# Kernel optimization log

Measured on AMD Instinct MI355X. Metric: run time of the kernel, lower is better.

Reference implementation:

```python
import jax, jax.numpy as jnp
import numpy as np
import math

D_MODEL = 2048
NUM_HEADS = 16
HEAD_DIM = D_MODEL // NUM_HEADS
B, QLEN, CACHE_LEN = 4, 512, 3584

def setup_inputs() -> dict:
    key = jax.random.key(0)
    ks = jax.random.split(key, 13)
    s = 0.02
    return {
        'query': jax.random.normal(ks[0], (B, QLEN, D_MODEL), jnp.float32),
        'key': jax.random.normal(ks[1], (B, QLEN, D_MODEL), jnp.float32),
        'value': jax.random.normal(ks[2], (B, QLEN, D_MODEL), jnp.float32),
        'cached_k': jax.random.normal(ks[3], (B, CACHE_LEN, D_MODEL), jnp.float32),
        'cached_v': jax.random.normal(ks[4], (B, CACHE_LEN, D_MODEL), jnp.float32),
        'wq': jax.random.normal(ks[5], (D_MODEL, D_MODEL), jnp.float32) * s,
        'bq': jnp.zeros((D_MODEL,), jnp.float32),
        'wk': jax.random.normal(ks[6], (D_MODEL, D_MODEL), jnp.float32) * s,
        'bk': jnp.zeros((D_MODEL,), jnp.float32),
        'wv': jax.random.normal(ks[7], (D_MODEL, D_MODEL), jnp.float32) * s,
        'bv': jnp.zeros((D_MODEL,), jnp.float32),
        'wo': jax.random.normal(ks[8], (D_MODEL, D_MODEL), jnp.float32) * s,
        'bo': jnp.zeros((D_MODEL,), jnp.float32),
    }

def _split_heads(x):
    b, s, _ = x.shape
    return x.reshape(b, s, NUM_HEADS, HEAD_DIM).transpose(0, 2, 1, 3)  # [b,h,s,d]

def reference(query, key, value, cached_k, cached_v, wq, bq, wk, bk, wv, bv, wo, bo):
    # projections (torch Linear: x @ W^T + b)
    Q = query @ wq.T + bq
    K_new = key @ wk.T + bk
    V_new = value @ wv.T + bv
    K = jnp.concatenate([cached_k, K_new], axis=1)  # [b, total, d_model]
    V = jnp.concatenate([cached_v, V_new], axis=1)
    seq_len = query.shape[1]
    total_len = K.shape[1]
    cache_len = total_len - seq_len
    Qh = _split_heads(Q)  # [b,h,q,d]
    Kh = _split_heads(K)  # [b,h,t,d]
    Vh = _split_heads(V)
    scale = math.sqrt(HEAD_DIM)
    scores = jnp.einsum('bhqd,bhtd->bhqt', Qh, Kh) / scale
    # causal mask with cache offset: query i attends to keys j <= cache_len + i
    q_idx = jnp.arange(seq_len)[:, None]
    k_idx = jnp.arange(total_len)[None, :]
    mask = k_idx > (q_idx + cache_len)  # True = masked
    scores = jnp.where(mask[None, None], -jnp.inf, scores)
    attn = jax.nn.softmax(scores, axis=-1)
    out = jnp.einsum('bhqt,bhtd->bhqd', attn, Vh)
    out = out.transpose(0, 2, 1, 3).reshape(query.shape[0], seq_len, D_MODEL)
    out = out @ wo.T + bo
    return out
```

## Files before the change

### kernel.cpp

```cpp
#include <hip/hip_runtime.h>

typedef _Float16 half8 __attribute__((ext_vector_type(8)));
typedef _Float16 half4v __attribute__((ext_vector_type(4)));
typedef float f32x4 __attribute__((ext_vector_type(4)));

#define NB 4
#define SQ 512
#define CL 3584
#define TT 4096
#define DM 2048
#define NH 16
#define DH 128

#define KSW(row, col) ((((row) * 128) + (col)) ^ ((((row) & 7) << 3)))
#define VSW(row, col) ((((row) * 64) + (col)) ^ ((((row) & 7) << 3)))
#define PSW(row, col) ((((row) * 64) + (col)) ^ ((((row) & 7) << 3)))

__device__ __forceinline__ void gl_lds16(const void* g, void* l) {
  __builtin_amdgcn_global_load_lds(
      (const __attribute__((address_space(1))) unsigned int*)g,
      (__attribute__((address_space(3))) unsigned int*)l, 16, 0, 0);
}

__global__ __launch_bounds__(256) void cvt_f16(
    const float* __restrict__ s0, const float* __restrict__ s1, const float* __restrict__ s2,
    _Float16* __restrict__ d0, _Float16* __restrict__ d1, _Float16* __restrict__ d2,
    int dstride)
{
  const float* s = blockIdx.y == 0 ? s0 : blockIdx.y == 1 ? s1 : s2;
  _Float16* d = blockIdx.y == 0 ? d0 : blockIdx.y == 1 ? d1 : d2;
  const int n4 = DM * DM / 4;
  for (int v = blockIdx.x * blockDim.x + threadIdx.x; v < n4;
       v += gridDim.x * blockDim.x) {
    float4 x = ((const float4*)s)[v];
    half4v h = { (_Float16)x.x, (_Float16)x.y, (_Float16)x.z, (_Float16)x.w };
    const int m = v >> 9, c = (v << 2) & 2047;
    *(half4v*)&d[(size_t)m * dstride + c] = h;
  }
}

__global__ __launch_bounds__(256) void convert_K(
    const float* __restrict__ ck, _Float16* __restrict__ K)
{
  const long long nvec = (long long)NB * CL * DM / 4;
  const int pb = CL * DM / 4;
  for (long long v = (long long)blockIdx.x * blockDim.x + threadIdx.x; v < nvec;
       v += (long long)gridDim.x * blockDim.x) {
    int b = (int)(v / pb);
    long long r = v - (long long)b * pb;
    float4 x = ((const float4*)ck)[v];
    half4v hx = { (_Float16)x.x, (_Float16)x.y, (_Float16)x.z, (_Float16)x.w };
    ((half4v*)K)[(long long)b * (TT * DM / 4) + r] = hx;
  }
}

__global__ __launch_bounds__(256) void transpose_V(
    const float* __restrict__ cv, _Float16* __restrict__ Vt)
{
  __shared__ _Float16 T[64][72];
  const int t0 = blockIdx.x * 64;
  const int dm0 = blockIdx.y * 64;
  const int b = blockIdx.z;
  const int tid = threadIdx.x;
  {
    const int tr = tid >> 2, c0 = (tid & 3) * 16;
    const float* src = cv + ((size_t)b * CL + t0 + tr) * DM + dm0 + c0;
    float4 a0 = ((const float4*)src)[0];
    float4 a1 = ((const float4*)src)[1];
    float4 a2 = ((const float4*)src)[2];
    float4 a3 = ((const float4*)src)[3];
    half8 h0 = { (_Float16)a0.x, (_Float16)a0.y, (_Float16)a0.z, (_Float16)a0.w,
                 (_Float16)a1.x, (_Float16)a1.y, (_Float16)a1.z, (_Float16)a1.w };
    half8 h1 = { (_Float16)a2.x, (_Float16)a2.y, (_Float16)a2.z, (_Float16)a2.w,
                 (_Float16)a3.x, (_Float16)a3.y, (_Float16)a3.z, (_Float16)a3.w };
    *(half8*)&T[tr][c0] = h0;
    *(half8*)&T[tr][c0 + 8] = h1;
  }
  __syncthreads();
  {
    const int dl = tid >> 2, tc = (tid & 3) * 16;
    const int h = dm0 >> 7, d = (dm0 & 127) + dl;
    half8 o0, o1;
#pragma unroll
    for (int i = 0; i < 8; ++i) o0[i] = T[tc + i][dl];
#pragma unroll
    for (int i = 0; i < 8; ++i) o1[i] = T[tc + 8 + i][dl];
    _Float16* dst = Vt + ((size_t)(b * NH + h) * DH + d) * TT + t0 + tc;
    *(half8*)dst = o0;
    *(half8*)(dst + 8) = o1;
  }
}

template<int MODE>
__global__ __launch_bounds__(512, 4) void mm16(
    const _Float16* __restrict__ A0, const _Float16* __restrict__ A1,
    const _Float16* __restrict__ A2, int astride,
    const _Float16* __restrict__ W0, const _Float16* __restrict__ W1,
    const _Float16* __restrict__ W2,
    const float* __restrict__ b0, const float* __restrict__ b1,
    const float* __restrict__ b2,
    _Float16* __restrict__ Qp, _Float16* __restrict__ Kc,
    _Float16* __restrict__ Vt, float* __restrict__ Co)
{
  __shared__ __align__(16) char smem[4 * 8192];
  char* Abuf = smem;
  char* Wbuf = smem + 2 * 8192;

  const int tid = threadIdx.x;
  const int bm = blockIdx.x, bn = blockIdx.y, z = blockIdx.z;
  const _Float16* Ain = z == 0 ? A0 : z == 1 ? A1 : A2;
  const _Float16* W   = z == 0 ? W0 : z == 1 ? W1 : W2;
  const float* bias   = z == 0 ? b0 : z == 1 ? b1 : b2;

  const int wid = tid >> 6, lane = tid & 63;
  const int wm = wid >> 2, wn = wid & 3;
  const int lr = lane & 15, lg = lane >> 4;

  f32x4 acc[4][2];
#pragma unroll
  for (int i = 0; i < 4; ++i)
#pragma unroll
    for (int j = 0; j < 2; ++j) acc[i][j] = (f32x4){0.f, 0.f, 0.f, 0.f};

  size_t aoff, woff;
  {
    const int o = wid * 1024 + lane * 16;
    const int prow = o >> 7, pb = o & 127;
    const int lb = pb ^ ((prow & 7) << 4);
    const int r = (prow << 1) | (lb >> 6), c = lb & 63;
    aoff = (size_t)(bm * 128 + r) * astride + c;
    woff = (size_t)(bn * 128 + r) * 4096 + c;
  }

  auto stage = [&](int kt, int buf) {
    gl_lds16((const char*)Ain + aoff + kt * 64, Abuf + buf * 8192 + wid * 1024);
    gl_lds16((const char*)W + woff + kt * 64, Wbuf + buf * 8192 + wid * 1024);
  };

  auto lds_addr = [](const char* base, int r, int cb) -> const char* {
    return base + ((r >> 1) << 7) + ((((r & 1) << 6) | cb) ^ (((r >> 1) & 7) << 4));
  };

  auto compute = [&](int buf) {
    const char* ab = Abuf + buf * 8192;
    const char* wb = Wbuf + buf * 8192;
    half8 af[4], bf[2];
#pragma unroll
    for (int i = 0; i < 4; ++i)
      af[i] = *(const half8*)lds_addr(ab, wm * 64 + i * 16 + lr, lg << 4);
#pragma unroll
    for (int j = 0; j < 2; ++j)
      bf[j] = *(const half8*)lds_addr(wb, wn * 32 + j * 16 + lr, lg << 4);
#pragma unroll
    for (int i = 0; i < 4; ++i)
#pragma unroll
      for (int j = 0; j < 2; ++j)
        acc[i][j] = __builtin_amdgcn_mfma_f32_16x16x32_f16(af[i], bf[j], acc[i][j], 0, 0, 0);
  };

  const int NKT = DM / 32;
  stage(0, 0);
  __syncthreads();
  for (int kt = 0; kt < NKT; ++kt) {
    if (kt + 1 < NKT) stage(kt + 1, (kt + 1) & 1);
    compute(kt & 1);
    __syncthreads();
  }

  const float qscale = 0.08838834764831845f * 1.4426950408889634f;
#pragma unroll
  for (int i = 0; i < 4; ++i) {
    const int m0 = bm * 128 + wm * 64 + i * 16 + lg * 4;
#pragma unroll
    for (int j = 0; j < 2; ++j) {
      const int gn = bn * 128 + wn * 32 + j * 16 + lr;
      const float bb = bias[gn];
      if constexpr (MODE == 1) {
#pragma unroll
        for (int r = 0; r < 4; ++r)
          Co[(size_t)(m0 + r) * DM + gn] = acc[i][j][r] + bb;
      } else {
        if (z == 0) {
#pragma unroll
          for (int r = 0; r < 4; ++r)
            Qp[(size_t)(m0 + r) * DM + gn] = (_Float16)((acc[i][j][r] + bb) * qscale);
        } else if (z == 1) {
          const int b = m0 >> 9;
#pragma unroll
          for (int r = 0; r < 4; ++r)
            Kc[((size_t)b * TT + CL + ((m0 + r) & 511)) * DM + gn] =
                (_Float16)(acc[i][j][r] + bb);
        } else {
          half4v hv;
#pragma unroll
          for (int r = 0; r < 4; ++r) hv[r] = (_Float16)(acc[i][j][r] + bb);
          const int b = m0 >> 9, t = CL + (m0 & 511);
          const int h = gn >> 7, d = gn & 127;
          *(half4v*)&Vt[((size_t)(b * NH + h) * DH + d) * TT + t] = hv;
        }
      }
    }
  }
}

__global__ __launch_bounds__(512) void attn_kernel(
    const _Float16* __restrict__ Qp, const _Float16* __restrict__ Kc,
    const _Float16* __restrict__ Vt, _Float16* __restrict__ O0,
    _Float16* __restrict__ O1, float2* __restrict__ ml)
{
  __shared__ _Float16 Ks[2][64 * 128];
  __shared__ _Float16 VTs[3][128 * 64];
  __shared__ _Float16 Ps[8][32 * 64];

  const int tid = threadIdx.x;
  const int lin = blockIdx.x;
  const int xcd = lin & 7, slot = lin >> 3;
  const int pair = xcd * 8 + (slot >> 2);
  const int rem = slot & 3;
  const int qb = rem >> 1, part = rem & 1;
  const int b = pair >> 4, h = pair & 15;

  const int wid = tid >> 6, lane = tid & 63;
  const int lr = lane & 15, lg = lane >> 4;
  const int qw = qb * 256 + wid * 32;

  half8 qf[2][4];
#pragma unroll
  for (int qs = 0; qs < 2; ++qs)
#pragma unroll
    for (int kk = 0; kk < 4; ++kk)
      qf[qs][kk] = *(const half8*)&Qp[(size_t)(b * SQ + qw + qs * 16 + lr) * DM +
                                      h * DH + kk * 32 + lg * 8];

  f32x4 zero = {0.f, 0.f, 0.f, 0.f};
  f32x4 acc[8][2];
#pragma unroll
  for (int d = 0; d < 8; ++d)
#pragma unroll
    for (int qs = 0; qs < 2; ++qs) acc[d][qs] = zero;
  float m_run[2] = {-1e30f, -1e30f}, l_run[2] = {0.f, 0.f};

  const int nt_full = (CL + qb * 256 + 256) / 64;
  const int halfn = nt_full >> 1;
  const int tbeg = part ? halfn : 0;
  const int nt = part ? (nt_full - halfn) : halfn;

  int ksrc[2], vsrc[2];
#pragma unroll
  for (int c = 0; c < 2; ++c) {
    const int p = c * 512 + wid * 64 + lane;
    { const int r = p >> 4, pg = p & 15, gc = pg ^ (r & 7);
      ksrc[c] = r * DM + gc * 8; }
    { const int d = p >> 3, pg = p & 7, gt = pg ^ (d & 7);
      vsrc[c] = d * TT + gt * 8; }
  }
  const _Float16* Kb = Kc + (size_t)b * TT * DM + h * DH;
  const _Float16* Vb = Vt + (size_t)(b * NH + h) * DH * TT;

  auto stage = [&](int tt, int kbuf, int vbuf) {
    const int t0 = (tbeg + tt) * 64;
#pragma unroll
    for (int c = 0; c < 2; ++c)
      gl_lds16(Kb + (size_t)t0 * DM + ksrc[c], &Ks[kbuf][(c * 512 + wid * 64) * 8]);
#pragma unroll
    for (int c = 0; c < 2; ++c)
      gl_lds16(Vb + t0 + vsrc[c], &VTs[vbuf][(c * 512 + wid * 64) * 8]);
  };

  auto qk = [&](int kbuf, f32x4 (*s)[2]) {
#pragma unroll
    for (int j = 0; j < 4; ++j)
#pragma unroll
      for (int qs = 0; qs < 2; ++qs) s[j][qs] = zero;
#pragma unroll
    for (int kk = 0; kk < 4; ++kk)
#pragma unroll
      for (int j = 0; j < 4; ++j) {
        half8 kb = *(const half8*)&Ks[kbuf][KSW(j * 16 + lr, kk * 32 + lg * 8)];
        s[j][0] = __builtin_amdgcn_mfma_f32_16x16x32_f16(kb, qf[0][kk], s[j][0], 0, 0, 0);
        s[j][1] = __builtin_amdgcn_mfma_f32_16x16x32_f16(kb, qf[1][kk], s[j][1], 0, 0, 0);
      }
  };

  auto mask_s = [&](int t0, f32x4 (*s)[2]) {
    if (t0 + 63 > CL + qw) {
#pragma unroll
      for (int j = 0; j < 4; ++j)
#pragma unroll
        for (int qs = 0; qs < 2; ++qs)
#pragma unroll
          for (int r = 0; r < 4; ++r)
            if (t0 + j * 16 + lg * 4 + r > CL + qw + qs * 16 + lr) s[j][qs][r] = -1e30f;
    }
  };

  auto softmax_step = [&](f32x4 (*s)[2]) {
    float mt[2];
#pragma unroll
    for (int qs = 0; qs < 2; ++qs) {
      float m = s[0][qs][0];
#pragma unroll
      for (int j = 0; j < 4; ++j)
#pragma unroll
        for (int r = 0; r < 4; ++r) m = fmaxf(m, s[j][qs][r]);
      mt[qs] = m;
    }
    if (!__all(mt[0] <= m_run[0] + 10.0f && mt[1] <= m_run[1] + 10.0f)) {
#pragma unroll
      for (int qs = 0; qs < 2; ++qs) {
        float m = fmaxf(mt[qs], __shfl_xor(mt[qs], 16));
        m = fmaxf(m, __shfl_xor(m, 32));
        const float mn = fmaxf(m_run[qs], m);
        const float fsc = exp2f(m_run[qs] - mn);
        m_run[qs] = mn;
        l_run[qs] *= fsc;
#pragma unroll
        for (int d = 0; d < 8; ++d)
#pragma unroll
          for (int r = 0; r < 4; ++r) acc[d][qs][r] *= fsc;
      }
    }
#pragma unroll
    for (int qs = 0; qs < 2; ++qs) {
      float ps = 0.f;
#pragma unroll
      for (int j = 0; j < 4; ++j) {
        float p0 = exp2f(s[j][qs][0] - m_run[qs]);
        float p1 = exp2f(s[j][qs][1] - m_run[qs]);
        float p2 = exp2f(s[j][qs][2] - m_run[qs]);
        float p3 = exp2f(s[j][qs][3] - m_run[qs]);
        ps += (p0 + p1) + (p2 + p3);
        half4v hp = { (_Float16)p0, (_Float16)p1, (_Float16)p2, (_Float16)p3 };
        *(half4v*)&Ps[wid][PSW(qs * 16 + lr, j * 16 + lg * 4)] = hp;
      }
      l_run[qs] += ps;
    }
  };

  auto pv = [&](int vbuf) {
#pragma unroll
    for (int kk = 0; kk < 2; ++kk) {
      half8 pf0 = *(const half8*)&Ps[wid][PSW(lr, kk * 32 + lg * 8)];
      half8 pf1 = *(const half8*)&Ps[wid][PSW(16 + lr, kk * 32 + lg * 8)];
#pragma unroll
      for (int d = 0; d < 8; ++d) {
        half8 vf = *(const half8*)&VTs[vbuf][VSW(d * 16 + lr, kk * 32 + lg * 8)];
        acc[d][0] = __builtin_amdgcn_mfma_f32_16x16x32_f16(vf, pf0, acc[d][0], 0, 0, 0);
        acc[d][1] = __builtin_amdgcn_mfma_f32_16x16x32_f16(vf, pf1, acc[d][1], 0, 0, 0);
      }
    }
  };

  f32x4 sp[4][2], sc[4][2];

  stage(0, 0, 0);
  __syncthreads();
  stage(1, 1, 1);
  qk(0, sp);
  mask_s(tbeg * 64, sp);

  for (int t = 1; t < nt; ++t) {
    __syncthreads();
    if (t + 1 < nt) stage(t + 1, (t + 1) & 1, (t + 1) % 3);
    qk(t & 1, sc);
    softmax_step(sp);
    pv((t - 1) % 3);
    mask_s((tbeg + t) * 64, sc);
#pragma unroll
    for (int j = 0; j < 4; ++j)
#pragma unroll
      for (int qs = 0; qs < 2; ++qs) sp[j][qs] = sc[j][qs];
  }
  softmax_step(sp);
  pv((nt - 1) % 3);

  _Float16* Od = part ? O1 : O0;
#pragma unroll
  for (int qs = 0; qs < 2; ++qs) {
    float lt = l_run[qs] + __shfl_xor(l_run[qs], 16);
    lt += __shfl_xor(lt, 32);
    const float inv = 1.0f / lt;
#pragma unroll
    for (int d = 0; d < 8; ++d) {
      half4v hv;
#pragma unroll
      for (int r = 0; r < 4; ++r) hv[r] = (_Float16)(acc[d][qs][r] * inv);
      *(half4v*)&Od[(size_t)(b * SQ + qw + qs * 16 + lr) * DM + h * DH + d * 16 + lg * 4] = hv;
    }
    if (lg == 0) {
      float2 e; e.x = m_run[qs]; e.y = lt;
      ml[part * (64 * SQ) + ((b * NH + h) * SQ) + qw + qs * 16 + lr] = e;
    }
  }
}

__global__ __launch_bounds__(256) void combine(
    _Float16* __restrict__ AO, const _Float16* __restrict__ O1,
    const float2* __restrict__ ml)
{
  const int idx = blockIdx.x * 256 + threadIdx.x;
  const int row = idx >> 8;
  const int col0 = (idx & 255) * 8;
  const int b = row >> 9, q = row & 511, h = col0 >> 7;
  const float2 e0 = ml[(b * NH + h) * SQ + q];
  const float2 e1 = ml[64 * SQ + (b * NH + h) * SQ + q];
  const float m = fmaxf(e0.x, e1.x);
  float w0 = e0.y * exp2f(e0.x - m);
  float w1 = e1.y * exp2f(e1.x - m);
  const float inv = 1.0f / (w0 + w1);
  w0 *= inv; w1 *= inv;
  const size_t o = (size_t)row * DM + col0;
  half8 a = *(const half8*)&AO[o];
  half8 c = *(const half8*)&O1[o];
  half8 r;
#pragma unroll
  for (int i = 0; i < 8; ++i)
    r[i] = (_Float16)(w0 * (float)a[i] + w1 * (float)c[i]);
  *(half8*)&AO[o] = r;
}

extern "C" void kernel_launch(void* const* d_in, const int* in_sizes, int n_in,
                              void* d_out, int out_size, void* d_ws, size_t ws_size,
                              hipStream_t stream) {
  const float* query = (const float*)d_in[0];
  const float* key   = (const float*)d_in[1];
  const float* value = (const float*)d_in[2];
  const float* ck    = (const float*)d_in[3];
  const float* cv    = (const float*)d_in[4];
  const float* wq = (const float*)d_in[5];
  const float* bq = (const float*)d_in[6];
  const float* wk = (const float*)d_in[7];
  const float* bk = (const float*)d_in[8];
  const float* wv = (const float*)d_in[9];
  const float* bv = (const float*)d_in[10];
  const float* wo = (const float*)d_in[11];
  const float* bo = (const float*)d_in[12];

  char* ws = (char*)d_ws;
  _Float16* Kc = (_Float16*)ws;
  _Float16* Vt = (_Float16*)(ws + 67108864);
  _Float16* Qp = (_Float16*)(ws + 134217728);
  _Float16* AO = (_Float16*)(ws + 142606336);

  _Float16* O1s = (_Float16*)d_out;
  float2* mls = (float2*)((char*)d_out + 8388608);

  _Float16* wqh = Kc;
  _Float16* wkh = Kc + 8388608;
  _Float16* wvh = Kc + 16777216;
  _Float16* qh = Vt;
  _Float16* kh = Vt + 2048 * 4096;
  _Float16* vh = Vt + 4096 * 4096;
  _Float16* woh = Qp;

  cvt_f16<<<dim3(512, 3), 256, 0, stream>>>(query, key, value, qh, kh, vh, 4096);
  cvt_f16<<<dim3(512, 3), 256, 0, stream>>>(wq, wk, wv, wqh, wkh, wvh, 2048);
  mm16<0><<<dim3(16, 16, 3), 512, 0, stream>>>(
      qh, kh, vh, 8192, wqh, wkh, wvh, bq, bk, bv, Qp, Kc, Vt, nullptr);
  convert_K<<<2048, 256, 0, stream>>>(ck, Kc);
  transpose_V<<<dim3(CL / 64, DM / 64, NB), 256, 0, stream>>>(cv, Vt);
  attn_kernel<<<256, 512, 0, stream>>>(Qp, Kc, Vt, AO, O1s, mls);
  combine<<<2048, 256, 0, stream>>>(AO, O1s, mls);
  cvt_f16<<<dim3(512, 1), 256, 0, stream>>>(wo, wo, wo, woh, woh, woh, 2048);
  mm16<1><<<dim3(16, 16, 1), 512, 0, stream>>>(
      AO, AO, AO, 4096, woh, woh, woh, bo, bo, bo, nullptr, nullptr, nullptr,
      (float*)d_out);
}
```

Measured before the change: 319.8 us.

## Split attention into 256-thread blocks with simpler double-buffered loop and setprio

The attention kernel moves from 256 blocks of 512 threads (256 queries each) to 512 blocks of 256 threads (128 queries each). The software pipeline that overlapped the next tile's QK with the current softmax/PV, along with the triple-buffered V, is replaced by a plain double-buffered loop. That loop wraps its MFMA sections in s_setprio and applies the causal mask only in the second key half. The smaller LDS footprint should let two blocks share a CU so barriers and phases interleave across blocks, at the risk of losing the explicit intra-wave overlap of softmax and matrix work.

After: 383.2 us. +19.8%, slower.

```diff
diff --git a/kernel.cpp b/kernel.cpp
--- a/kernel.cpp
+++ b/kernel.cpp
@@ -203,26 +203,26 @@
   }
 }
 
-__global__ __launch_bounds__(512) void attn_kernel(
+__global__ __launch_bounds__(256) void attn_kernel(
     const _Float16* __restrict__ Qp, const _Float16* __restrict__ Kc,
     const _Float16* __restrict__ Vt, _Float16* __restrict__ O0,
     _Float16* __restrict__ O1, float2* __restrict__ ml)
 {
   __shared__ _Float16 Ks[2][64 * 128];
-  __shared__ _Float16 VTs[3][128 * 64];
-  __shared__ _Float16 Ps[8][32 * 64];
+  __shared__ _Float16 VTs[2][128 * 64];
+  __shared__ _Float16 Ps[4][32 * 64];
 
   const int tid = threadIdx.x;
   const int lin = blockIdx.x;
   const int xcd = lin & 7, slot = lin >> 3;
-  const int pair = xcd * 8 + (slot >> 2);
-  const int rem = slot & 3;
+  const int pair = xcd * 8 + (slot >> 3);
+  const int rem = slot & 7;
   const int qb = rem >> 1, part = rem & 1;
   const int b = pair >> 4, h = pair & 15;
 
   const int wid = tid >> 6, lane = tid & 63;
   const int lr = lane & 15, lg = lane >> 4;
-  const int qw = qb * 256 + wid * 32;
+  const int qw = qb * 128 + wid * 32;
 
   half8 qf[2][4];
 #pragma unroll
@@ -240,15 +240,15 @@
     for (int qs = 0; qs < 2; ++qs) acc[d][qs] = zero;
   float m_run[2] = {-1e30f, -1e30f}, l_run[2] = {0.f, 0.f};
 
-  const int nt_full = (CL + qb * 256 + 256) / 64;
+  const int nt_full = (CL + qb * 128 + 128) / 64;
   const int halfn = nt_full >> 1;
   const int tbeg = part ? halfn : 0;
   const int nt = part ? (nt_full - halfn) : halfn;
 
-  int ksrc[2], vsrc[2];
-#pragma unroll
-  for (int c = 0; c < 2; ++c) {
-    const int p = c * 512 + wid * 64 + lane;
+  int ksrc[4], vsrc[4];
+#pragma unroll
+  for (int c = 0; c < 4; ++c) {
+    const int p = c * 256 + tid;
     { const int r = p >> 4, pg = p & 15, gc = pg ^ (r & 7);
       ksrc[c] = r * DM + gc * 8; }
     { const int d = p >> 3, pg = p & 7, gt = pg ^ (d & 7);
@@ -257,44 +257,53 @@
   const _Float16* Kb = Kc + (size_t)b * TT * DM + h * DH;
   const _Float16* Vb = Vt + (size_t)(b * NH + h) * DH * TT;
 
-  auto stage = [&](int tt, int kbuf, int vbuf) {
+  auto stage = [&](int tt, int buf) {
     const int t0 = (tbeg + tt) * 64;
 #pragma unroll
-    for (int c = 0; c < 2; ++c)
-      gl_lds16(Kb + (size_t)t0 * DM + ksrc[c], &Ks[kbuf][(c * 512 + wid * 64) * 8]);
-#pragma unroll
-    for (int c = 0; c < 2; ++c)
-      gl_lds16(Vb + t0 + vsrc[c], &VTs[vbuf][(c * 512 + wid * 64) * 8]);
+    for (int c = 0; c < 4; ++c)
+      gl_lds16(Kb + (size_t)t0 * DM + ksrc[c], &Ks[buf][(c * 256 + tid) * 8]);
+#pragma unroll
+    for (int c = 0; c < 4; ++c)
+      gl_lds16(Vb + t0 + vsrc[c], &VTs[buf][(c * 256 + tid) * 8]);
   };
 
-  auto qk = [&](int kbuf, f32x4 (*s)[2]) {
+  f32x4 s[4][2];
+
+  stage(0, 0);
+  __syncthreads();
+
+  for (int t = 0; t < nt; ++t) {
+    const int cur = t & 1;
+    if (t + 1 < nt) stage(t + 1, cur ^ 1);
+
 #pragma unroll
     for (int j = 0; j < 4; ++j)
 #pragma unroll
       for (int qs = 0; qs < 2; ++qs) s[j][qs] = zero;
+    __builtin_amdgcn_s_setprio(1);
 #pragma unroll
     for (int kk = 0; kk < 4; ++kk)
 #pragma unroll
       for (int j = 0; j < 4; ++j) {
-        half8 kb = *(const half8*)&Ks[kbuf][KSW(j * 16 + lr, kk * 32 + lg * 8)];
+        half8 kb = *(const half8*)&Ks[cur][KSW(j * 16 + lr, kk * 32 + lg * 8)];
         s[j][0] = __builtin_amdgcn_mfma_f32_16x16x32_f16(kb, qf[0][kk], s[j][0], 0, 0, 0);
         s[j][1] = __builtin_amdgcn_mfma_f32_16x16x32_f16(kb, qf[1][kk], s[j][1], 0, 0, 0);
       }
-  };
-
-  auto mask_s = [&](int t0, f32x4 (*s)[2]) {
-    if (t0 + 63 > CL + qw) {
-#pragma unroll
-      for (int j = 0; j < 4; ++j)
-#pragma unroll
-        for (int qs = 0; qs < 2; ++qs)
-#pragma unroll
-          for (int r = 0; r < 4; ++r)
-            if (t0 + j * 16 + lg * 4 + r > CL + qw + qs * 16 + lr) s[j][qs][r] = -1e30f;
-    }
-  };
-
-  auto softmax_step = [&](f32x4 (*s)[2]) {
+    __builtin_amdgcn_s_setprio(0);
+
+    if (part) {
+      const int t0 = (tbeg + t) * 64;
+      if (t0 + 63 > CL + qw) {
+#pragma unroll
+        for (int j = 0; j < 4; ++j)
+#pragma unroll
+          for (int qs = 0; qs < 2; ++qs)
+#pragma unroll
+            for (int r = 0; r < 4; ++r)
+              if (t0 + j * 16 + lg * 4 + r > CL + qw + qs * 16 + lr) s[j][qs][r] = -1e30f;
+      }
+    }
+
     float mt[2];
 #pragma unroll
     for (int qs = 0; qs < 2; ++qs) {
@@ -335,44 +344,23 @@
       }
       l_run[qs] += ps;
     }
-  };
-
-  auto pv = [&](int vbuf) {
+
+    __builtin_amdgcn_s_setprio(1);
 #pragma unroll
     for (int kk = 0; kk < 2; ++kk) {
       half8 pf0 = *(const half8*)&Ps[wid][PSW(lr, kk * 32 + lg * 8)];
       half8 pf1 = *(const half8*)&Ps[wid][PSW(16 + lr, kk * 32 + lg * 8)];
 #pragma unroll
       for (int d = 0; d < 8; ++d) {
-        half8 vf = *(const half8*)&VTs[vbuf][VSW(d * 16 + lr, kk * 32 + lg * 8)];
+        half8 vf = *(const half8*)&VTs[cur][VSW(d * 16 + lr, kk * 32 + lg * 8)];
         acc[d][0] = __builtin_amdgcn_mfma_f32_16x16x32_f16(vf, pf0, acc[d][0], 0, 0, 0);
         acc[d][1] = __builtin_amdgcn_mfma_f32_16x16x32_f16(vf, pf1, acc[d][1], 0, 0, 0);
       }
     }
-  };
-
-  f32x4 sp[4][2], sc[4][2];
-
-  stage(0, 0, 0);
-  __syncthreads();
-  stage(1, 1, 1);
-  qk(0, sp);
-  mask_s(tbeg * 64, sp);
-
-  for (int t = 1; t < nt; ++t) {
+    __builtin_amdgcn_s_setprio(0);
+
     __syncthreads();
-    if (t + 1 < nt) stage(t + 1, (t + 1) & 1, (t + 1) % 3);
-    qk(t & 1, sc);
-    softmax_step(sp);
-    pv((t - 1) % 3);
-    mask_s((tbeg + t) * 64, sc);
-#pragma unroll
-    for (int j = 0; j < 4; ++j)
-#pragma unroll
-      for (int qs = 0; qs < 2; ++qs) sp[j][qs] = sc[j][qs];
-  }
-  softmax_step(sp);
-  pv((nt - 1) % 3);
+  }
 
   _Float16* Od = part ? O1 : O0;
 #pragma unroll
@@ -459,7 +447,7 @@
       qh, kh, vh, 8192, wqh, wkh, wvh, bq, bk, bv, Qp, Kc, Vt, nullptr);
   convert_K<<<2048, 256, 0, stream>>>(ck, Kc);
   transpose_V<<<dim3(CL / 64, DM / 64, NB), 256, 0, stream>>>(cv, Vt);
-  attn_kernel<<<256, 512, 0, stream>>>(Qp, Kc, Vt, AO, O1s, mls);
+  attn_kernel<<<512, 256, 0, stream>>>(Qp, Kc, Vt, AO, O1s, mls);
   combine<<<2048, 256, 0, stream>>>(AO, O1s, mls);
   cvt_f16<<<dim3(512, 1), 256, 0, stream>>>(wo, wo, wo, woh, woh, woh, 2048);
   mm16<1><<<dim3(16, 16, 1), 512, 0, stream>>>(
```
